# Optimization experiments

Measured on AMD Instinct MI355X. Metric: run time of the kernel, lower is better.

Reference implementation:

```python
import jax, jax.numpy as jnp
import numpy as np

B, C, Z, H, W = 1, 64, 8, 32, 32
C8 = C // 8


def setup_inputs() -> dict:
    key = jax.random.key(0)
    ks = jax.random.split(key, 8)
    shp = (B, C, Z, H, W)
    return {
        "x1": jax.random.normal(ks[0], shp, dtype=jnp.float32),
        "x2": jax.random.normal(ks[1], shp, dtype=jnp.float32),
        # 1x1x1 Conv3d weights are pointwise channel matmuls: [out, in]
        "Wf": jax.random.normal(ks[2], (C8, C), dtype=jnp.float32) * (1.0 / np.sqrt(C)),
        "bf": jnp.zeros((C8,), dtype=jnp.float32),
        "Wg": jax.random.normal(ks[3], (C8, C), dtype=jnp.float32) * (1.0 / np.sqrt(C)),
        "bg": jnp.zeros((C8,), dtype=jnp.float32),
        "Wh1": jax.random.normal(ks[4], (C, C), dtype=jnp.float32) * (1.0 / np.sqrt(C)),
        "bh1": jnp.zeros((C,), dtype=jnp.float32),
        "Wh2": jax.random.normal(ks[5], (C, C), dtype=jnp.float32) * (1.0 / np.sqrt(C)),
        "bh2": jnp.zeros((C,), dtype=jnp.float32),
        "gamma1": jax.random.uniform(ks[6], (1,), dtype=jnp.float32),
        "gamma2": jax.random.uniform(ks[7], (1,), dtype=jnp.float32),
    }


def _attend(x, Wf, bf, Wg, bg, Wh, bh, gamma):
    b, c, z, h, w = x.shape
    n = z * h * w
    xf = x.reshape(b, c, n)                                  # [B, C, N]
    f = jnp.einsum('oc,bcn->bno', Wf, xf) + bf               # [B, N, C//8]
    g = jnp.einsum('oc,bcn->bon', Wg, xf) + bg[:, None]      # [B, C//8, N]
    # unscaled attention logits, softmax over last dim (torch dim=2)
    att = jax.nn.softmax(jnp.einsum('bnk,bkm->bnm', f, g), axis=2)  # [B, N, N]
    v = jnp.einsum('oc,bcn->bon', Wh, xf) + bh[:, None]      # [B, C, N]
    sa = jnp.einsum('bcn,bnm->bcm', v, att).reshape(x.shape)  # h @ attention
    return gamma * sa + x


def reference(x1, x2, Wf, bf, Wg, bg, Wh1, bh1, Wh2, bh2, gamma1, gamma2):
    y1 = _attend(x1, Wf, bf, Wg, bg, Wh1, bh1, gamma1)
    y2 = _attend(x2, Wf, bf, Wg, bg, Wh2, bh2, gamma2)
    return (y1, y2)
```

## Files before the change

kernel.cpp:

```cpp
#include <hip/hip_runtime.h>
#include <math.h>

#define N 8192
#define WSP (80*N)
#define OFF_G (8*N)
#define OFF_T (16*N)

typedef __attribute__((ext_vector_type(8)))  short bf16x8;
typedef __attribute__((ext_vector_type(4)))  float f32x4;
typedef __attribute__((ext_vector_type(16))) float f32x16;

#define ZERO16 ((f32x16){0.f,0.f,0.f,0.f,0.f,0.f,0.f,0.f,0.f,0.f,0.f,0.f,0.f,0.f,0.f,0.f})

#if defined(__has_builtin)
#  if __has_builtin(__builtin_amdgcn_exp2f)
#    define EXP2(x) __builtin_amdgcn_exp2f(x)
#  endif
#endif
#ifndef EXP2
#  define EXP2(x) exp2f(x)
#endif

__device__ __forceinline__ unsigned short bf_hi(float x) {
    union { float f; unsigned u; } v; v.f = x;
    unsigned r = v.u + 0x7fffu + ((v.u >> 16) & 1u);
    return (unsigned short)(r >> 16);
}
__device__ __forceinline__ float bf_f(unsigned short h) {
    union { float f; unsigned u; } v; v.u = ((unsigned)h) << 16;
    return v.f;
}
__device__ __forceinline__ unsigned pack_hi16(unsigned i1, unsigned i0) {
#if defined(__has_builtin) && __has_builtin(__builtin_amdgcn_perm)
    return __builtin_amdgcn_perm(i1, i0, 0x07060302u);
#else
    return (i1 & 0xffff0000u) | (i0 >> 16);
#endif
}

__device__ __forceinline__ void xcd_map(int lin, int& a, int& idx) {
    int xcd = lin & 7;
    a   = xcd >> 2;
    idx = (xcd & 3) | ((lin >> 3) << 2);
}

__global__ __launch_bounds__(512) void prep_kernel(
    const float* __restrict__ x1, const float* __restrict__ x2,
    const float* __restrict__ Wf, const float* __restrict__ bf,
    const float* __restrict__ Wg, const float* __restrict__ bg,
    const float* __restrict__ Wh1, const float* __restrict__ bh1,
    const float* __restrict__ Wh2, const float* __restrict__ bh2,
    float* __restrict__ ws)
{
    int a, bidx;
    xcd_map(blockIdx.x + (int)gridDim.x * blockIdx.y, a, bidx);
    const float* x  = a ? x2  : x1;
    const float* Wh = a ? Wh2 : Wh1;
    const float* bh = a ? bh2 : bh1;
    float* base = ws + (size_t)a * WSP;
    unsigned short* F16 = (unsigned short*)base;
    unsigned short* G16 = (unsigned short*)(base + OFF_G);
    float* vb = base + OFF_T;

    __shared__ float xs[64][33];
    __shared__ float Wlds[80][64];
    __shared__ float blds[80];

    const int n0 = bidx * 32;
    const int t  = threadIdx.x;
    for (int i = t; i < 64*32; i += 512) {
        int c = i >> 5, j = i & 31;
        xs[c][j] = x[(size_t)c*N + n0 + j];
    }
    for (int i = t; i < 80*64; i += 512) {
        int o = i >> 6, c = i & 63;
        float v;
        if (o < 8)       v = Wf[o*64 + c];
        else if (o < 16) v = Wg[(o-8)*64 + c];
        else             v = Wh[(o-16)*64 + c];
        Wlds[o][c] = v;
    }
    if (t < 80) blds[t] = (t < 8) ? bf[t] : (t < 16) ? bg[t-8] : bh[t-16];
    __syncthreads();

    const int j  = t & 31;
    const int og = t >> 5;
    float s[5];
    #pragma unroll
    for (int k = 0; k < 5; ++k) s[k] = blds[og + 16*k];
    #pragma unroll 8
    for (int c = 0; c < 64; ++c) {
        float xc = xs[c][j];
        #pragma unroll
        for (int k = 0; k < 5; ++k) s[k] += Wlds[og + 16*k][c] * xc;
    }
    const float LOG2E = 1.44269504088896340736f;
    #pragma unroll
    for (int k = 0; k < 5; ++k) {
        int o = og + 16*k;
        if (o < 8) {
            float v = s[k] * LOG2E;
            unsigned short h = bf_hi(v);
            F16[(size_t)(n0+j)*16 + o]     = h;
            F16[(size_t)(n0+j)*16 + 8 + o] = bf_hi(v - bf_f(h));
        } else if (o < 16) {
            float v = s[k];
            unsigned short h = bf_hi(v);
            G16[(size_t)(n0+j)*16 + (o-8)]     = h;
            G16[(size_t)(n0+j)*16 + 8 + (o-8)] = bf_hi(v - bf_f(h));
        } else {
            vb[(size_t)(n0+j)*64 + (o-16)] = s[k];
        }
    }
}

__global__ __launch_bounds__(512, 4) void rownorm_kernel(float* __restrict__ ws)
{
    int a, bidx;
    xcd_map(blockIdx.x + (int)gridDim.x * blockIdx.y, a, bidx);
    float* base = ws + (size_t)a * WSP;
    const unsigned short* F16 = (const unsigned short*)base;
    const unsigned short* G16 = (const unsigned short*)(base + OFF_G);
    float* vb = base + OFF_T;
    const int n0 = bidx * 32;
    const int t  = threadIdx.x;
    const int w = t >> 6, lane = t & 63, l31 = lane & 31, hi = lane >> 5;

    __shared__ float vbs[32][64];
    __shared__ float lsum[8][32];
    __shared__ float linv[32];

    {
        const f32x4* vp = (const f32x4*)(vb + (size_t)n0*64);
        f32x4 v = __builtin_nontemporal_load(vp + t);
        *(f32x4*)&vbs[t >> 4][(t & 15) * 4] = v;
    }

    const bf16x8 A1 = *(const bf16x8*)(F16 + (size_t)(n0 + l31)*16 + hi*8);
    const bf16x8 z8 = {0,0,0,0,0,0,0,0};
    const bf16x8 A2 = hi ? z8 : A1;

    f32x16 sum = ZERO16;
    for (int ms = w*(N/8); ms < (w+1)*(N/8); ms += 64) {
        const bf16x8 B1a = *(const bf16x8*)(G16 + (size_t)(ms + l31)*16);
        const bf16x8 B2a = *(const bf16x8*)(G16 + (size_t)(ms + l31)*16 + 8);
        const bf16x8 B1b = *(const bf16x8*)(G16 + (size_t)(ms + 32 + l31)*16);
        const bf16x8 B2b = *(const bf16x8*)(G16 + (size_t)(ms + 32 + l31)*16 + 8);
        f32x16 Sa = __builtin_amdgcn_mfma_f32_32x32x16_bf16(A1, B1a, ZERO16, 0, 0, 0);
        Sa = __builtin_amdgcn_mfma_f32_32x32x16_bf16(A2, B2a, Sa, 0, 0, 0);
        f32x16 Sb = __builtin_amdgcn_mfma_f32_32x32x16_bf16(A1, B1b, ZERO16, 0, 0, 0);
        Sb = __builtin_amdgcn_mfma_f32_32x32x16_bf16(A2, B2b, Sb, 0, 0, 0);
        #pragma unroll
        for (int r = 0; r < 16; ++r) sum[r] += EXP2(Sa[r]) + EXP2(Sb[r]);
    }
    #pragma unroll
    for (int r = 0; r < 16; ++r) {
        float v = sum[r];
        v += __shfl_xor(v, 1, 64);
        v += __shfl_xor(v, 2, 64);
        v += __shfl_xor(v, 4, 64);
        v += __shfl_xor(v, 8, 64);
        v += __shfl_xor(v, 16, 64);
        sum[r] = v;
    }
    if (l31 == 0) {
        #pragma unroll
        for (int r = 0; r < 16; ++r) {
            int n = (r & 3) + 8*(r >> 2) + 4*hi;
            lsum[w][n] = sum[r];
        }
    }
    __syncthreads();
    if (t < 32) {
        float v = 0.f;
        #pragma unroll
        for (int ww = 0; ww < 8; ++ww) v += lsum[ww][t];
        linv[t] = 1.0f / v;
    }
    __syncthreads();

    if (t < 256) {
        const int c = t & 63, kkg = t >> 6;
        bf16x8 H, L;
        #pragma unroll
        for (int jj = 0; jj < 8; ++jj) {
            int n_rd = (kkg >> 1)*16 + 4*(kkg & 1) + (jj & 3) + 8*((jj >> 2) & 1);
            float v = vbs[n_rd][c] * linv[n_rd];
            unsigned short h = bf_hi(v);
            H[jj] = (short)h;
            L[jj] = (short)bf_hi(v - bf_f(h));
        }
        unsigned short* tile = (unsigned short*)(base + OFF_T) + (size_t)(n0 >> 5) * 4096;
        unsigned short* tp = tile + c*32 + kkg*8;
        *(bf16x8*)tp          = H;
        *(bf16x8*)(tp + 2048) = L;
    }
}

__global__ __launch_bounds__(512, 2) void attn_kernel(
    const float* __restrict__ x1, const float* __restrict__ x2,
    const float* __restrict__ ga1, const float* __restrict__ ga2,
    const float* __restrict__ ws, float* __restrict__ out_)
{
    int a, bidx;
    xcd_map(blockIdx.x + (int)gridDim.x * blockIdx.y, a, bidx);
    const float* x = a ? x2 : x1;
    const float gamma = a ? ga2[0] : ga1[0];
    const float* base = ws + (size_t)a * WSP;
    const unsigned short* F16 = (const unsigned short*)base;
    const unsigned short* G16 = (const unsigned short*)(base + OFF_G);
    const unsigned short* tiles = (const unsigned short*)(base + OFF_T);
    float* out = out_ + (size_t)a * ((size_t)64 * N);

    const int m0 = bidx * 64;
    const int t = threadIdx.x;
    const int w = t >> 6, lane = t & 63, l31 = lane & 31, hi = lane >> 5;

    const bf16x8 z8 = {0,0,0,0,0,0,0,0};
    bf16x8 Bh0, Bl0, Bh1, Bl1;
    {
        const unsigned short* gp0 = G16 + (size_t)(m0 + l31)*16;
        const unsigned short* gp1 = G16 + (size_t)(m0 + 32 + l31)*16;
        Bh0 = *(const bf16x8*)gp0;
        Bl0 = hi ? z8 : *(const bf16x8*)(gp0 + 8);
        Bh1 = *(const bf16x8*)gp1;
        Bl1 = hi ? z8 : *(const bf16x8*)(gp1 + 8);
    }

    f32x16 accA = ZERO16, accB = ZERO16;
    f32x16 accC = ZERO16, accD = ZERO16;

    const int kbeg = w * (N/8);
    const int KM = (N/8) - 1;

    bf16x8 Acur, Anxt;
    bf16x8 AH[4], AL[4];

    Acur = *(const bf16x8*)(F16 + (size_t)(kbeg + l31)*16 + hi*8);
    Anxt = *(const bf16x8*)(F16 + (size_t)(kbeg + 32 + l31)*16 + hi*8);
    {
        const unsigned short* tb = tiles + (size_t)(kbeg >> 5) * 4096;
        #pragma unroll
        for (int kp = 0; kp < 2; ++kp)
            #pragma unroll
            for (int ct = 0; ct < 2; ++ct) {
                const unsigned short* tc = tb + (ct*32 + l31)*32 + kp*16 + hi*8;
                AH[kp*2+ct] = *(const bf16x8*)tc;
                AL[kp*2+ct] = *(const bf16x8*)(tc + 2048);
            }
    }

    for (int it = 0; it < 32; ++it) {
        f32x16 S0 = __builtin_amdgcn_mfma_f32_32x32x16_bf16(Acur, Bh0, ZERO16, 0, 0, 0);
        f32x16 S1 = __builtin_amdgcn_mfma_f32_32x32x16_bf16(Acur, Bh1, ZERO16, 0, 0, 0);
        S0 = __builtin_amdgcn_mfma_f32_32x32x16_bf16(Acur, Bl0, S0, 0, 0, 0);
        S1 = __builtin_amdgcn_mfma_f32_32x32x16_bf16(Acur, Bl1, S1, 0, 0, 0);
        Acur = Anxt;
        Anxt = *(const bf16x8*)(F16 + (size_t)(kbeg + (((it+2)*32) & KM) + l31)*16 + hi*8);

        union BU { bf16x8 v; unsigned u[4]; };
        BU pH0[2], pL0[2], pH1[2], pL1[2];
        #pragma unroll
        for (int kp = 0; kp < 2; ++kp)
            #pragma unroll
            for (int d = 0; d < 4; ++d) {
                float q0 = EXP2(S0[kp*8 + 2*d]);
                float q1 = EXP2(S0[kp*8 + 2*d + 1]);
                unsigned i0 = __float_as_uint(q0), i1 = __float_as_uint(q1);
                pH0[kp].u[d] = pack_hi16(i1, i0);
                unsigned r0 = __float_as_uint(q0 - __uint_as_float(i0 & 0xffff0000u));
                unsigned r1 = __float_as_uint(q1 - __uint_as_float(i1 & 0xffff0000u));
                pL0[kp].u[d] = pack_hi16(r1, r0);

                float q2 = EXP2(S1[kp*8 + 2*d]);
                float q3 = EXP2(S1[kp*8 + 2*d + 1]);
                unsigned i2 = __float_as_uint(q2), i3 = __float_as_uint(q3);
                pH1[kp].u[d] = pack_hi16(i3, i2);
                unsigned r2 = __float_as_uint(q2 - __uint_as_float(i2 & 0xffff0000u));
                unsigned r3 = __float_as_uint(q3 - __uint_as_float(i3 & 0xffff0000u));
                pL1[kp].u[d] = pack_hi16(r3, r2);
            }

        #pragma unroll
        for (int kp = 0; kp < 2; ++kp) {
            accA = __builtin_amdgcn_mfma_f32_32x32x16_bf16(AH[kp*2+0], pH0[kp].v, accA, 0, 0, 0);
            accC = __builtin_amdgcn_mfma_f32_32x32x16_bf16(AH[kp*2+0], pH1[kp].v, accC, 0, 0, 0);
            accA = __builtin_amdgcn_mfma_f32_32x32x16_bf16(AH[kp*2+0], pL0[kp].v, accA, 0, 0, 0);
            accC = __builtin_amdgcn_mfma_f32_32x32x16_bf16(AH[kp*2+0], pL1[kp].v, accC, 0, 0, 0);
            accA = __builtin_amdgcn_mfma_f32_32x32x16_bf16(AL[kp*2+0], pH0[kp].v, accA, 0, 0, 0);
            accC = __builtin_amdgcn_mfma_f32_32x32x16_bf16(AL[kp*2+0], pH1[kp].v, accC, 0, 0, 0);
            accB = __builtin_amdgcn_mfma_f32_32x32x16_bf16(AH[kp*2+1], pH0[kp].v, accB, 0, 0, 0);
            accD = __builtin_amdgcn_mfma_f32_32x32x16_bf16(AH[kp*2+1], pH1[kp].v, accD, 0, 0, 0);
            accB = __builtin_amdgcn_mfma_f32_32x32x16_bf16(AH[kp*2+1], pL0[kp].v, accB, 0, 0, 0);
            accD = __builtin_amdgcn_mfma_f32_32x32x16_bf16(AH[kp*2+1], pL1[kp].v, accD, 0, 0, 0);
            accB = __builtin_amdgcn_mfma_f32_32x32x16_bf16(AL[kp*2+1], pH0[kp].v, accB, 0, 0, 0);
            accD = __builtin_amdgcn_mfma_f32_32x32x16_bf16(AL[kp*2+1], pH1[kp].v, accD, 0, 0, 0);
        }

        {
            const unsigned short* tb = tiles
                + (size_t)((kbeg + (((it+1)*32) & KM)) >> 5) * 4096;
            #pragma unroll
            for (int kp = 0; kp < 2; ++kp)
                #pragma unroll
                for (int ct = 0; ct < 2; ++ct) {
                    const unsigned short* tc = tb + (ct*32 + l31)*32 + kp*16 + hi*8;
                    AH[kp*2+ct] = *(const bf16x8*)tc;
                    AL[kp*2+ct] = *(const bf16x8*)(tc + 2048);
                }
        }
    }

    __shared__ float red[64][65];
    for (int ww = 0; ww < 8; ++ww) {
        if (w == ww) {
            #pragma unroll
            for (int mg = 0; mg < 2; ++mg)
                #pragma unroll
                for (int ct = 0; ct < 2; ++ct) {
                    const f32x16& A = mg ? (ct ? accD : accC) : (ct ? accB : accA);
                    #pragma unroll
                    for (int r = 0; r < 16; ++r) {
                        int c = ct*32 + (r & 3) + 8*(r >> 2) + 4*hi;
                        int m = mg*32 + l31;
                        if (ww == 0) red[c][m]  = A[r];
                        else         red[c][m] += A[r];
                    }
                }
        }
        __syncthreads();
    }
    #pragma unroll
    for (int i = 0; i < 8; ++i) {
        int e = t + 512*i;
        int c = e >> 6, m = e & 63;
        size_t gi = (size_t)c*N + m0 + m;
        float xv = __builtin_nontemporal_load(x + gi);
        __builtin_nontemporal_store(gamma * red[c][m] + xv, out + gi);
    }
}

extern "C" void kernel_launch(void* const* d_in, const int* in_sizes, int n_in,
                              void* d_out, int out_size, void* d_ws, size_t ws_size,
                              hipStream_t stream)
{
    (void)in_sizes; (void)n_in; (void)out_size; (void)ws_size;
    const float* x1  = (const float*)d_in[0];
    const float* x2  = (const float*)d_in[1];
    const float* Wf  = (const float*)d_in[2];
    const float* bf  = (const float*)d_in[3];
    const float* Wg  = (const float*)d_in[4];
    const float* bg  = (const float*)d_in[5];
    const float* Wh1 = (const float*)d_in[6];
    const float* bh1 = (const float*)d_in[7];
    const float* Wh2 = (const float*)d_in[8];
    const float* bh2 = (const float*)d_in[9];
    const float* g1  = (const float*)d_in[10];
    const float* g2  = (const float*)d_in[11];
    float* out = (float*)d_out;
    float* ws  = (float*)d_ws;

    prep_kernel   <<<dim3(N/32, 2), dim3(512), 0, stream>>>(x1,x2,Wf,bf,Wg,bg,Wh1,bh1,Wh2,bh2,ws);
    rownorm_kernel<<<dim3(N/32, 2), dim3(512), 0, stream>>>(ws);
    attn_kernel   <<<dim3(N/64, 2), dim3(512), 0, stream>>>(x1,x2,g1,g2,ws,out);
}
```

Before: 170.3 us.

## Software-pipeline logit MFMAs with exp work and vectorize prep projection

In the main attention kernel, the QK^T MFMAs for the next key block are now issued in the middle of the current block's exp/pack and PV MFMA sequence, so matrix and vector work overlap. That section also runs at raised wave priority. The row-sum kernel is rewritten the same way, computing the next S while exponentiating the current one with prefetched G loads. The prep kernel transposes the x tile in LDS and uses float4 LDS and global loads for the weights and the channel dot products. This raises register pressure and may change code scheduling or occupancy.

```diff
diff --git a/kernel.cpp b/kernel.cpp
--- a/kernel.cpp
+++ b/kernel.cpp
@@ -62,23 +62,20 @@
     unsigned short* G16 = (unsigned short*)(base + OFF_G);
     float* vb = base + OFF_T;
 
-    __shared__ float xs[64][33];
-    __shared__ float Wlds[80][64];
+    __shared__ __align__(16) float xs[32][68];
+    __shared__ __align__(16) float Wlds[80][64];
     __shared__ float blds[80];
 
     const int n0 = bidx * 32;
     const int t  = threadIdx.x;
     for (int i = t; i < 64*32; i += 512) {
         int c = i >> 5, j = i & 31;
-        xs[c][j] = x[(size_t)c*N + n0 + j];
-    }
-    for (int i = t; i < 80*64; i += 512) {
-        int o = i >> 6, c = i & 63;
-        float v;
-        if (o < 8)       v = Wf[o*64 + c];
-        else if (o < 16) v = Wg[(o-8)*64 + c];
-        else             v = Wh[(o-16)*64 + c];
-        Wlds[o][c] = v;
+        xs[j][c] = x[(size_t)c*N + n0 + j];
+    }
+    for (int i4 = t; i4 < 80*16; i4 += 512) {
+        int o = i4 >> 4, c4 = i4 & 15;
+        const float* src = (o < 8) ? (Wf + o*64) : (o < 16) ? (Wg + (o-8)*64) : (Wh + (o-16)*64);
+        *(f32x4*)&Wlds[o][c4*4] = *(const f32x4*)(src + c4*4);
     }
     if (t < 80) blds[t] = (t < 8) ? bf[t] : (t < 16) ? bg[t-8] : bh[t-16];
     __syncthreads();
@@ -88,11 +85,18 @@
     float s[5];
     #pragma unroll
     for (int k = 0; k < 5; ++k) s[k] = blds[og + 16*k];
-    #pragma unroll 8
-    for (int c = 0; c < 64; ++c) {
-        float xc = xs[c][j];
-        #pragma unroll
-        for (int k = 0; k < 5; ++k) s[k] += Wlds[og + 16*k][c] * xc;
+    const f32x4* xrow = (const f32x4*)&xs[j][0];
+    #pragma unroll 4
+    for (int c4 = 0; c4 < 16; ++c4) {
+        const f32x4 xv = xrow[c4];
+        #pragma unroll
+        for (int k = 0; k < 5; ++k) {
+            const f32x4 wv = *(const f32x4*)&Wlds[og + 16*k][c4*4];
+            s[k] += wv.x * xv.x;
+            s[k] += wv.y * xv.y;
+            s[k] += wv.z * xv.z;
+            s[k] += wv.w * xv.w;
+        }
     }
     const float LOG2E = 1.44269504088896340736f;
     #pragma unroll
@@ -140,18 +144,29 @@
     const bf16x8 z8 = {0,0,0,0,0,0,0,0};
     const bf16x8 A2 = hi ? z8 : A1;
 
-    f32x16 sum = ZERO16;
-    for (int ms = w*(N/8); ms < (w+1)*(N/8); ms += 64) {
-        const bf16x8 B1a = *(const bf16x8*)(G16 + (size_t)(ms + l31)*16);
-        const bf16x8 B2a = *(const bf16x8*)(G16 + (size_t)(ms + l31)*16 + 8);
-        const bf16x8 B1b = *(const bf16x8*)(G16 + (size_t)(ms + 32 + l31)*16);
-        const bf16x8 B2b = *(const bf16x8*)(G16 + (size_t)(ms + 32 + l31)*16 + 8);
-        f32x16 Sa = __builtin_amdgcn_mfma_f32_32x32x16_bf16(A1, B1a, ZERO16, 0, 0, 0);
-        Sa = __builtin_amdgcn_mfma_f32_32x32x16_bf16(A2, B2a, Sa, 0, 0, 0);
-        f32x16 Sb = __builtin_amdgcn_mfma_f32_32x32x16_bf16(A1, B1b, ZERO16, 0, 0, 0);
-        Sb = __builtin_amdgcn_mfma_f32_32x32x16_bf16(A2, B2b, Sb, 0, 0, 0);
-        #pragma unroll
-        for (int r = 0; r < 16; ++r) sum[r] += EXP2(Sa[r]) + EXP2(Sb[r]);
+    const int mb = w * (N/8);
+    const int MM = (N/8) - 1;
+    bf16x8 B1, B2;
+    f32x16 S, sum = ZERO16;
+
+    B1 = *(const bf16x8*)(G16 + (size_t)(mb + l31)*16);
+    B2 = *(const bf16x8*)(G16 + (size_t)(mb + l31)*16 + 8);
+    S = __builtin_amdgcn_mfma_f32_32x32x16_bf16(A1, B1, ZERO16, 0, 0, 0);
+    S = __builtin_amdgcn_mfma_f32_32x32x16_bf16(A2, B2, S, 0, 0, 0);
+    B1 = *(const bf16x8*)(G16 + (size_t)(mb + 32 + l31)*16);
+    B2 = *(const bf16x8*)(G16 + (size_t)(mb + 32 + l31)*16 + 8);
+
+    for (int it = 0; it < 32; ++it) {
+        f32x16 Sn = __builtin_amdgcn_mfma_f32_32x32x16_bf16(A1, B1, ZERO16, 0, 0, 0);
+        Sn = __builtin_amdgcn_mfma_f32_32x32x16_bf16(A2, B2, Sn, 0, 0, 0);
+        {
+            const size_t mrow = mb + (((it+2)*32) & MM) + l31;
+            B1 = *(const bf16x8*)(G16 + mrow*16);
+            B2 = *(const bf16x8*)(G16 + mrow*16 + 8);
+        }
+        #pragma unroll
+        for (int r = 0; r < 16; ++r) sum[r] += EXP2(S[r]);
+        S = Sn;
     }
     #pragma unroll
     for (int r = 0; r < 16; ++r) {
@@ -233,11 +248,16 @@
     const int kbeg = w * (N/8);
     const int KM = (N/8) - 1;
 
-    bf16x8 Acur, Anxt;
+    bf16x8 A;
     bf16x8 AH[4], AL[4];
-
-    Acur = *(const bf16x8*)(F16 + (size_t)(kbeg + l31)*16 + hi*8);
-    Anxt = *(const bf16x8*)(F16 + (size_t)(kbeg + 32 + l31)*16 + hi*8);
+    f32x16 S0, S1;
+
+    A = *(const bf16x8*)(F16 + (size_t)(kbeg + l31)*16 + hi*8);
+    S0 = __builtin_amdgcn_mfma_f32_32x32x16_bf16(A, Bh0, ZERO16, 0, 0, 0);
+    S1 = __builtin_amdgcn_mfma_f32_32x32x16_bf16(A, Bh1, ZERO16, 0, 0, 0);
+    S0 = __builtin_amdgcn_mfma_f32_32x32x16_bf16(A, Bl0, S0, 0, 0, 0);
+    S1 = __builtin_amdgcn_mfma_f32_32x32x16_bf16(A, Bl1, S1, 0, 0, 0);
+    A = *(const bf16x8*)(F16 + (size_t)(kbeg + 32 + l31)*16 + hi*8);
     {
         const unsigned short* tb = tiles + (size_t)(kbeg >> 5) * 4096;
         #pragma unroll
@@ -250,53 +270,80 @@
             }
     }
 
+    union BU { bf16x8 v; unsigned u[4]; };
+
     for (int it = 0; it < 32; ++it) {
-        f32x16 S0 = __builtin_amdgcn_mfma_f32_32x32x16_bf16(Acur, Bh0, ZERO16, 0, 0, 0);
-        f32x16 S1 = __builtin_amdgcn_mfma_f32_32x32x16_bf16(Acur, Bh1, ZERO16, 0, 0, 0);
-        S0 = __builtin_amdgcn_mfma_f32_32x32x16_bf16(Acur, Bl0, S0, 0, 0, 0);
-        S1 = __builtin_amdgcn_mfma_f32_32x32x16_bf16(Acur, Bl1, S1, 0, 0, 0);
-        Acur = Anxt;
-        Anxt = *(const bf16x8*)(F16 + (size_t)(kbeg + (((it+2)*32) & KM) + l31)*16 + hi*8);
-
-        union BU { bf16x8 v; unsigned u[4]; };
-        BU pH0[2], pL0[2], pH1[2], pL1[2];
-        #pragma unroll
-        for (int kp = 0; kp < 2; ++kp)
+        __builtin_amdgcn_s_setprio(1);
+        {
+            BU pH0, pL0, pH1, pL1;
             #pragma unroll
             for (int d = 0; d < 4; ++d) {
-                float q0 = EXP2(S0[kp*8 + 2*d]);
-                float q1 = EXP2(S0[kp*8 + 2*d + 1]);
+                float q0 = EXP2(S0[2*d]);
+                float q1 = EXP2(S0[2*d + 1]);
                 unsigned i0 = __float_as_uint(q0), i1 = __float_as_uint(q1);
-                pH0[kp].u[d] = pack_hi16(i1, i0);
+                pH0.u[d] = pack_hi16(i1, i0);
                 unsigned r0 = __float_as_uint(q0 - __uint_as_float(i0 & 0xffff0000u));
                 unsigned r1 = __float_as_uint(q1 - __uint_as_float(i1 & 0xffff0000u));
-                pL0[kp].u[d] = pack_hi16(r1, r0);
-
-                float q2 = EXP2(S1[kp*8 + 2*d]);
-                float q3 = EXP2(S1[kp*8 + 2*d + 1]);
+                pL0.u[d] = pack_hi16(r1, r0);
+                float q2 = EXP2(S1[2*d]);
+                float q3 = EXP2(S1[2*d + 1]);
                 unsigned i2 = __float_as_uint(q2), i3 = __float_as_uint(q3);
-                pH1[kp].u[d] = pack_hi16(i3, i2);
+                pH1.u[d] = pack_hi16(i3, i2);
                 unsigned r2 = __float_as_uint(q2 - __uint_as_float(i2 & 0xffff0000u));
                 unsigned r3 = __float_as_uint(q3 - __uint_as_float(i3 & 0xffff0000u));
-                pL1[kp].u[d] = pack_hi16(r3, r2);
+                pL1.u[d] = pack_hi16(r3, r2);
             }
-
-        #pragma unroll
-        for (int kp = 0; kp < 2; ++kp) {
-            accA = __builtin_amdgcn_mfma_f32_32x32x16_bf16(AH[kp*2+0], pH0[kp].v, accA, 0, 0, 0);
-            accC = __builtin_amdgcn_mfma_f32_32x32x16_bf16(AH[kp*2+0], pH1[kp].v, accC, 0, 0, 0);
-            accA = __builtin_amdgcn_mfma_f32_32x32x16_bf16(AH[kp*2+0], pL0[kp].v, accA, 0, 0, 0);
-            accC = __builtin_amdgcn_mfma_f32_32x32x16_bf16(AH[kp*2+0], pL1[kp].v, accC, 0, 0, 0);
-            accA = __builtin_amdgcn_mfma_f32_32x32x16_bf16(AL[kp*2+0], pH0[kp].v, accA, 0, 0, 0);
-            accC = __builtin_amdgcn_mfma_f32_32x32x16_bf16(AL[kp*2+0], pH1[kp].v, accC, 0, 0, 0);
-            accB = __builtin_amdgcn_mfma_f32_32x32x16_bf16(AH[kp*2+1], pH0[kp].v, accB, 0, 0, 0);
-            accD = __builtin_amdgcn_mfma_f32_32x32x16_bf16(AH[kp*2+1], pH1[kp].v, accD, 0, 0, 0);
-            accB = __builtin_amdgcn_mfma_f32_32x32x16_bf16(AH[kp*2+1], pL0[kp].v, accB, 0, 0, 0);
-            accD = __builtin_amdgcn_mfma_f32_32x32x16_bf16(AH[kp*2+1], pL1[kp].v, accD, 0, 0, 0);
-            accB = __builtin_amdgcn_mfma_f32_32x32x16_bf16(AL[kp*2+1], pH0[kp].v, accB, 0, 0, 0);
-            accD = __builtin_amdgcn_mfma_f32_32x32x16_bf16(AL[kp*2+1], pH1[kp].v, accD, 0, 0, 0);
-        }
-
+            accA = __builtin_amdgcn_mfma_f32_32x32x16_bf16(AH[0], pH0.v, accA, 0, 0, 0);
+            accC = __builtin_amdgcn_mfma_f32_32x32x16_bf16(AH[0], pH1.v, accC, 0, 0, 0);
+            accA = __builtin_amdgcn_mfma_f32_32x32x16_bf16(AH[0], pL0.v, accA, 0, 0, 0);
+            accC = __builtin_amdgcn_mfma_f32_32x32x16_bf16(AH[0], pL1.v, accC, 0, 0, 0);
+            accA = __builtin_amdgcn_mfma_f32_32x32x16_bf16(AL[0], pH0.v, accA, 0, 0, 0);
+            accC = __builtin_amdgcn_mfma_f32_32x32x16_bf16(AL[0], pH1.v, accC, 0, 0, 0);
+            accB = __builtin_amdgcn_mfma_f32_32x32x16_bf16(AH[1], pH0.v, accB, 0, 0, 0);
+            accD = __builtin_amdgcn_mfma_f32_32x32x16_bf16(AH[1], pH1.v, accD, 0, 0, 0);
+            accB = __builtin_amdgcn_mfma_f32_32x32x16_bf16(AH[1], pL0.v, accB, 0, 0, 0);
+            accD = __builtin_amdgcn_mfma_f32_32x32x16_bf16(AH[1], pL1.v, accD, 0, 0, 0);
+            accB = __builtin_amdgcn_mfma_f32_32x32x16_bf16(AL[1], pH0.v, accB, 0, 0, 0);
+            accD = __builtin_amdgcn_mfma_f32_32x32x16_bf16(AL[1], pH1.v, accD, 0, 0, 0);
+        }
+        {
+            BU pH0, pL0, pH1, pL1;
+            #pragma unroll
+            for (int d = 0; d < 4; ++d) {
+                float q0 = EXP2(S0[8 + 2*d]);
+                float q1 = EXP2(S0[8 + 2*d + 1]);
+                unsigned i0 = __float_as_uint(q0), i1 = __float_as_uint(q1);
+                pH0.u[d] = pack_hi16(i1, i0);
+                unsigned r0 = __float_as_uint(q0 - __uint_as_float(i0 & 0xffff0000u));
+                unsigned r1 = __float_as_uint(q1 - __uint_as_float(i1 & 0xffff0000u));
+                pL0.u[d] = pack_hi16(r1, r0);
+                float q2 = EXP2(S1[8 + 2*d]);
+                float q3 = EXP2(S1[8 + 2*d + 1]);
+                unsigned i2 = __float_as_uint(q2), i3 = __float_as_uint(q3);
+                pH1.u[d] = pack_hi16(i3, i2);
+                unsigned r2 = __float_as_uint(q2 - __uint_as_float(i2 & 0xffff0000u));
+                unsigned r3 = __float_as_uint(q3 - __uint_as_float(i3 & 0xffff0000u));
+                pL1.u[d] = pack_hi16(r3, r2);
+            }
+            S0 = __builtin_amdgcn_mfma_f32_32x32x16_bf16(A, Bh0, ZERO16, 0, 0, 0);
+            S1 = __builtin_amdgcn_mfma_f32_32x32x16_bf16(A, Bh1, ZERO16, 0, 0, 0);
+            S0 = __builtin_amdgcn_mfma_f32_32x32x16_bf16(A, Bl0, S0, 0, 0, 0);
+            S1 = __builtin_amdgcn_mfma_f32_32x32x16_bf16(A, Bl1, S1, 0, 0, 0);
+            A = *(const bf16x8*)(F16 + (size_t)(kbeg + (((it+2)*32) & KM) + l31)*16 + hi*8);
+            accA = __builtin_amdgcn_mfma_f32_32x32x16_bf16(AH[2], pH0.v, accA, 0, 0, 0);
+            accC = __builtin_amdgcn_mfma_f32_32x32x16_bf16(AH[2], pH1.v, accC, 0, 0, 0);
+            accA = __builtin_amdgcn_mfma_f32_32x32x16_bf16(AH[2], pL0.v, accA, 0, 0, 0);
+            accC = __builtin_amdgcn_mfma_f32_32x32x16_bf16(AH[2], pL1.v, accC, 0, 0, 0);
+            accA = __builtin_amdgcn_mfma_f32_32x32x16_bf16(AL[2], pH0.v, accA, 0, 0, 0);
+            accC = __builtin_amdgcn_mfma_f32_32x32x16_bf16(AL[2], pH1.v, accC, 0, 0, 0);
+            accB = __builtin_amdgcn_mfma_f32_32x32x16_bf16(AH[3], pH0.v, accB, 0, 0, 0);
+            accD = __builtin_amdgcn_mfma_f32_32x32x16_bf16(AH[3], pH1.v, accD, 0, 0, 0);
+            accB = __builtin_amdgcn_mfma_f32_32x32x16_bf16(AH[3], pL0.v, accB, 0, 0, 0);
+            accD = __builtin_amdgcn_mfma_f32_32x32x16_bf16(AH[3], pL1.v, accD, 0, 0, 0);
+            accB = __builtin_amdgcn_mfma_f32_32x32x16_bf16(AL[3], pH0.v, accB, 0, 0, 0);
+            accD = __builtin_amdgcn_mfma_f32_32x32x16_bf16(AL[3], pH1.v, accD, 0, 0, 0);
+        }
+        __builtin_amdgcn_s_setprio(0);
         {
             const unsigned short* tb = tiles
                 + (size_t)((kbeg + (((it+1)*32) & KM)) >> 5) * 4096;
@@ -318,13 +365,13 @@
             for (int mg = 0; mg < 2; ++mg)
                 #pragma unroll
                 for (int ct = 0; ct < 2; ++ct) {
-                    const f32x16& A = mg ? (ct ? accD : accC) : (ct ? accB : accA);
+                    const f32x16& Ac = mg ? (ct ? accD : accC) : (ct ? accB : accA);
                     #pragma unroll
                     for (int r = 0; r < 16; ++r) {
                         int c = ct*32 + (r & 3) + 8*(r >> 2) + 4*hi;
                         int m = mg*32 + l31;
-                        if (ww == 0) red[c][m]  = A[r];
-                        else         red[c][m] += A[r];
+                        if (ww == 0) red[c][m]  = Ac[r];
+                        else         red[c][m] += Ac[r];
                     }
                 }
         }
```

After: 168.3 us. No clear change (-1.1%).

## Transpose prep LDS layouts, store V channel-major, software-pipeline rownorm loads

Applied to the files above, without the earlier changes.

The prep kernel now keeps x transposed in LDS and reads it and the weights as float4 vectors, and loads weights with vector global loads. V is written channel-major, so prep stores coalesce along n, and rownorm reads it back with a transposed, padded LDS scatter. The rownorm loop processes one 32-column block per iteration and prefetches the next G block while computing exp2 on the previous logits, to hide load latency. The tile-write thread mapping also changes. The costs are extra LDS bank-conflict risk and a loop that keeps fewer independent MFMAs in flight.

```diff
diff --git a/kernel.cpp b/kernel.cpp
--- a/kernel.cpp
+++ b/kernel.cpp
@@ -62,23 +62,20 @@
     unsigned short* G16 = (unsigned short*)(base + OFF_G);
     float* vb = base + OFF_T;
 
-    __shared__ float xs[64][33];
-    __shared__ float Wlds[80][64];
+    __shared__ __align__(16) float xs[32][68];
+    __shared__ __align__(16) float Wlds[80][64];
     __shared__ float blds[80];
 
     const int n0 = bidx * 32;
     const int t  = threadIdx.x;
     for (int i = t; i < 64*32; i += 512) {
         int c = i >> 5, j = i & 31;
-        xs[c][j] = x[(size_t)c*N + n0 + j];
-    }
-    for (int i = t; i < 80*64; i += 512) {
-        int o = i >> 6, c = i & 63;
-        float v;
-        if (o < 8)       v = Wf[o*64 + c];
-        else if (o < 16) v = Wg[(o-8)*64 + c];
-        else             v = Wh[(o-16)*64 + c];
-        Wlds[o][c] = v;
+        xs[j][c] = x[(size_t)c*N + n0 + j];
+    }
+    for (int i4 = t; i4 < 80*16; i4 += 512) {
+        int o = i4 >> 4, c4 = i4 & 15;
+        const float* src = (o < 8) ? (Wf + o*64) : (o < 16) ? (Wg + (o-8)*64) : (Wh + (o-16)*64);
+        *(f32x4*)&Wlds[o][c4*4] = *(const f32x4*)(src + c4*4);
     }
     if (t < 80) blds[t] = (t < 8) ? bf[t] : (t < 16) ? bg[t-8] : bh[t-16];
     __syncthreads();
@@ -88,11 +85,18 @@
     float s[5];
     #pragma unroll
     for (int k = 0; k < 5; ++k) s[k] = blds[og + 16*k];
-    #pragma unroll 8
-    for (int c = 0; c < 64; ++c) {
-        float xc = xs[c][j];
-        #pragma unroll
-        for (int k = 0; k < 5; ++k) s[k] += Wlds[og + 16*k][c] * xc;
+    const f32x4* xrow = (const f32x4*)&xs[j][0];
+    #pragma unroll 4
+    for (int c4 = 0; c4 < 16; ++c4) {
+        const f32x4 xv = xrow[c4];
+        #pragma unroll
+        for (int k = 0; k < 5; ++k) {
+            const f32x4 wv = *(const f32x4*)&Wlds[og + 16*k][c4*4];
+            s[k] += wv.x * xv.x;
+            s[k] += wv.y * xv.y;
+            s[k] += wv.z * xv.z;
+            s[k] += wv.w * xv.w;
+        }
     }
     const float LOG2E = 1.44269504088896340736f;
     #pragma unroll
@@ -109,7 +113,7 @@
             G16[(size_t)(n0+j)*16 + (o-8)]     = h;
             G16[(size_t)(n0+j)*16 + 8 + (o-8)] = bf_hi(v - bf_f(h));
         } else {
-            vb[(size_t)(n0+j)*64 + (o-16)] = s[k];
+            vb[(size_t)(o-16)*N + n0 + j] = s[k];
         }
     }
 }
@@ -126,32 +130,47 @@
     const int t  = threadIdx.x;
     const int w = t >> 6, lane = t & 63, l31 = lane & 31, hi = lane >> 5;
 
-    __shared__ float vbs[32][64];
+    __shared__ float vbs[32][65];
     __shared__ float lsum[8][32];
     __shared__ float linv[32];
 
     {
-        const f32x4* vp = (const f32x4*)(vb + (size_t)n0*64);
-        f32x4 v = __builtin_nontemporal_load(vp + t);
-        *(f32x4*)&vbs[t >> 4][(t & 15) * 4] = v;
+        const int c = t >> 3, g = t & 7;
+        const f32x4 v = __builtin_nontemporal_load(
+            (const f32x4*)(vb + (size_t)c*N + n0 + g*4));
+        vbs[g*4+0][c] = v.x;
+        vbs[g*4+1][c] = v.y;
+        vbs[g*4+2][c] = v.z;
+        vbs[g*4+3][c] = v.w;
     }
 
     const bf16x8 A1 = *(const bf16x8*)(F16 + (size_t)(n0 + l31)*16 + hi*8);
     const bf16x8 z8 = {0,0,0,0,0,0,0,0};
     const bf16x8 A2 = hi ? z8 : A1;
 
-    f32x16 sum = ZERO16;
-    for (int ms = w*(N/8); ms < (w+1)*(N/8); ms += 64) {
-        const bf16x8 B1a = *(const bf16x8*)(G16 + (size_t)(ms + l31)*16);
-        const bf16x8 B2a = *(const bf16x8*)(G16 + (size_t)(ms + l31)*16 + 8);
-        const bf16x8 B1b = *(const bf16x8*)(G16 + (size_t)(ms + 32 + l31)*16);
-        const bf16x8 B2b = *(const bf16x8*)(G16 + (size_t)(ms + 32 + l31)*16 + 8);
-        f32x16 Sa = __builtin_amdgcn_mfma_f32_32x32x16_bf16(A1, B1a, ZERO16, 0, 0, 0);
-        Sa = __builtin_amdgcn_mfma_f32_32x32x16_bf16(A2, B2a, Sa, 0, 0, 0);
-        f32x16 Sb = __builtin_amdgcn_mfma_f32_32x32x16_bf16(A1, B1b, ZERO16, 0, 0, 0);
-        Sb = __builtin_amdgcn_mfma_f32_32x32x16_bf16(A2, B2b, Sb, 0, 0, 0);
-        #pragma unroll
-        for (int r = 0; r < 16; ++r) sum[r] += EXP2(Sa[r]) + EXP2(Sb[r]);
+    const int mb = w * (N/8);
+    const int MM = (N/8) - 1;
+    bf16x8 B1, B2;
+    f32x16 S, sum = ZERO16;
+
+    B1 = *(const bf16x8*)(G16 + (size_t)(mb + l31)*16);
+    B2 = *(const bf16x8*)(G16 + (size_t)(mb + l31)*16 + 8);
+    S = __builtin_amdgcn_mfma_f32_32x32x16_bf16(A1, B1, ZERO16, 0, 0, 0);
+    S = __builtin_amdgcn_mfma_f32_32x32x16_bf16(A2, B2, S, 0, 0, 0);
+    B1 = *(const bf16x8*)(G16 + (size_t)(mb + 32 + l31)*16);
+    B2 = *(const bf16x8*)(G16 + (size_t)(mb + 32 + l31)*16 + 8);
+
+    for (int it = 0; it < 32; ++it) {
+        f32x16 Sn = __builtin_amdgcn_mfma_f32_32x32x16_bf16(A1, B1, ZERO16, 0, 0, 0);
+        Sn = __builtin_amdgcn_mfma_f32_32x32x16_bf16(A2, B2, Sn, 0, 0, 0);
+        {
+            const size_t mrow = mb + (((it+2)*32) & MM) + l31;
+            B1 = *(const bf16x8*)(G16 + mrow*16);
+            B2 = *(const bf16x8*)(G16 + mrow*16 + 8);
+        }
+        #pragma unroll
+        for (int r = 0; r < 16; ++r) sum[r] += EXP2(S[r]);
+        S = Sn;
     }
     #pragma unroll
     for (int r = 0; r < 16; ++r) {
@@ -180,7 +199,7 @@
     __syncthreads();
 
     if (t < 256) {
-        const int c = t & 63, kkg = t >> 6;
+        const int c = t >> 2, kkg = t & 3;
         bf16x8 H, L;
         #pragma unroll
         for (int jj = 0; jj < 8; ++jj) {
@@ -318,13 +337,13 @@
             for (int mg = 0; mg < 2; ++mg)
                 #pragma unroll
                 for (int ct = 0; ct < 2; ++ct) {
-                    const f32x16& A = mg ? (ct ? accD : accC) : (ct ? accB : accA);
+                    const f32x16& Ac = mg ? (ct ? accD : accC) : (ct ? accB : accA);
                     #pragma unroll
                     for (int r = 0; r < 16; ++r) {
                         int c = ct*32 + (r & 3) + 8*(r >> 2) + 4*hi;
                         int m = mg*32 + l31;
-                        if (ww == 0) red[c][m]  = A[r];
-                        else         red[c][m] += A[r];
+                        if (ww == 0) red[c][m]  = Ac[r];
+                        else         red[c][m] += Ac[r];
                     }
                 }
         }
```

Measured after the change: 169.2 us. No clear change (-0.6%).
